# Performance work log

Measured on AMD Instinct MI355X. Metric: run time of the kernel, lower is better.

Reference implementation:

```python
import jax, jax.numpy as jnp
import numpy as np

B, L, H, C, K, S = 8, 336, 192, 321, 16, 8
H2 = H // 2 + 1            # rfft bins of pred_len
OUT = H2 * (2 * K + 1)     # FilterFactory out_dim


def _instance_norm(t):
    mu = t.mean(-1, keepdims=True)
    tc = t - mu
    std = jnp.sqrt((tc * tc).mean(-1, keepdims=True) + 1e-8)
    return tc / std, mu, std


def setup_inputs() -> dict:
    key = jax.random.key(0)
    ks = jax.random.split(key, 16)
    x = jax.random.normal(ks[0], (B, L, C), jnp.float32)
    y_hat = jax.random.normal(ks[1], (B, H, C), jnp.float32)
    leader_ids = jax.random.randint(ks[2], (B, C, K), 0, C)
    shift = jax.random.randint(ks[3], (B, C, K), 0, L)
    r = jax.random.normal(ks[4], (B, C, K), jnp.float32)
    temperature = jnp.ones((1,), jnp.float32)
    sl = 1.0 / np.sqrt(L)
    cls_w = jax.random.uniform(ks[5], (S, L), jnp.float32, -sl, sl)
    cls_bias = jax.random.uniform(ks[6], (S,), jnp.float32, -sl, sl)
    ss = 1.0 / np.sqrt(S)
    basic_state = jax.random.uniform(ks[7], (C, S), jnp.float32, -ss, ss)
    sk = 1.0 / np.sqrt(K)
    mh_w = jax.random.uniform(ks[8], (S, K * OUT), jnp.float32, -sk, sk)
    mh_b = jax.random.uniform(ks[9], (S, OUT), jnp.float32, -sk, sk)
    sm = 1.0 / np.sqrt(3 * H2)
    mix_w_real = jax.random.uniform(ks[10], (H2, 3 * H2), jnp.float32, -sm, sm)
    mix_w_imag = jax.random.uniform(ks[11], (H2, 3 * H2), jnp.float32, -sm, sm)
    mix_b_real = jax.random.uniform(ks[12], (H2,), jnp.float32, -sm, sm)
    mix_b_imag = jax.random.uniform(ks[13], (H2,), jnp.float32, -sm, sm)
    return dict(x=x, y_hat=y_hat, leader_ids=leader_ids, shift=shift, r=r,
                temperature=temperature, cls_w=cls_w, cls_bias=cls_bias,
                basic_state=basic_state, mh_w=mh_w, mh_b=mh_b,
                mix_w_real=mix_w_real, mix_w_imag=mix_w_imag,
                mix_b_real=mix_b_real, mix_b_imag=mix_b_imag)


def reference(x, y_hat, leader_ids, shift, r, temperature, cls_w, cls_bias,
              basic_state, mh_w, mh_b, mix_w_real, mix_w_imag,
              mix_b_real, mix_b_imag):
    xc = jnp.transpose(x, (0, 2, 1))        # [B,C,L]
    yh = jnp.transpose(y_hat, (0, 2, 1))    # [B,C,H]
    xn, mu, std = _instance_norm(xc)
    yhn = (yh - mu) / std

    # ---- shifted leader gather (no-grad region in original) ----
    seq = jnp.concatenate([xn, yhn], -1)                                      # [B,C,L+H]
    lead = jnp.take_along_axis(seq[:, None], leader_ids[..., None], axis=2)   # [B,C,K,L+H]
    idx = jnp.arange(L, L + H)[None, None, None, :] - shift[..., None]        # [B,C,K,H]
    seq_shifted = jnp.take_along_axis(lead, idx, axis=-1)
    seq_shifted = jax.lax.stop_gradient(seq_shifted * jnp.sign(r)[..., None])

    # ---- temperature softmax over [1, |r|] ----
    ones = jnp.ones((xc.shape[0], C, 1), xc.dtype)
    rw = jax.nn.softmax(jnp.concatenate([ones, jnp.abs(r)], -1) / temperature, axis=-1)
    corr_feat = rw[..., 1:]                                                   # [B,C,K]

    # ---- FilterFactory: state-routed filters ----
    p = jax.nn.softmax(cls_bias + basic_state + jnp.einsum('bcl,sl->bcs', xc, cls_w), axis=-1)
    w = jnp.einsum('bcs,so->bco', p, mh_w).reshape(-1, C, K, OUT)
    b = jnp.einsum('bcs,so->bco', p, mh_b)
    filt = (jnp.einsum('bck,bcko->bco', corr_feat, w) + b).reshape(-1, C, 2 * K + 1, H2)

    # ---- FFT filter mixing ----
    yf = jnp.fft.rfft(yhn)                                  # [B,C,H2] complex64
    sf = jnp.fft.rfft(seq_shifted) * filt[:, :, :K]         # [B,C,K,H2]
    df = (sf - yf[:, :, None]) * filt[:, :, K:-1]
    yf2 = yf * filt[:, :, -1]
    mix_in = jnp.concatenate([sf.sum(2), df.sum(2), yf2], -1)  # [B,C,3*H2]
    mix_w = mix_w_real + 1j * mix_w_imag
    mix_b = mix_b_real + 1j * mix_b_imag
    y = yhn + jnp.fft.irfft(mix_in @ mix_w.T + mix_b, n=H)
    y = y * std + mu
    return jnp.transpose(y, (0, 2, 1))                       # [B,H,C]
```

## Files before the change

### kernel.cpp

```cpp
#include <hip/hip_runtime.h>
#include <math.h>

#define B_ 8
#define L_ 336
#define H_ 192
#define C_ 321
#define K_ 16
#define S_ 8
#define H2_ 97
#define OUT_ 3201
#define SEQLEN_ 528
#define BC_ (B_ * C_)
#define JD_ 136
#define MIXJ_ 291
#define NP_ 208
#define MPAD_ 43712
#define NBLK_ 683
#define KF_ 160
#define MPADF_ 2576
#define NPADF_ 3264
#define KMX_ 608
#define NMX_ 208
#define KIR_ 224
#define NIR_ 192

typedef float v2f __attribute__((ext_vector_type(2)));
typedef float v4f __attribute__((ext_vector_type(4)));
typedef __attribute__((ext_vector_type(8))) short bf16x8;
typedef __attribute__((ext_vector_type(4))) float f32x4;

#define TWO_PI_F 6.283185307179586f

static constexpr size_t OFF_SEQ    = 0;
static constexpr size_t OFF_MU     = OFF_SEQ + (size_t)BC_ * SEQLEN_;
static constexpr size_t OFF_STD    = OFF_MU + BC_;
static constexpr size_t OFF_BPHI   = (OFF_STD + BC_ + 3) & ~(size_t)3;
static constexpr size_t OFF_BPLO   = OFF_BPHI + (size_t)NP_ * 192 / 2;
static constexpr size_t OFF_UHI    = (OFF_BPLO + (size_t)NP_ * 192 / 2 + 3) & ~(size_t)3;
static constexpr size_t OFF_ULO    = OFF_UHI + (size_t)MPADF_ * KF_ / 2;
static constexpr size_t OFF_W2HI   = OFF_ULO + (size_t)MPADF_ * KF_ / 2;
static constexpr size_t OFF_W2LO   = OFF_W2HI + (size_t)NPADF_ * KF_ / 2;
static constexpr size_t OFF_ROWS   = OFF_W2LO + (size_t)NPADF_ * KF_ / 2;
static constexpr size_t OFF_ROWSLO = OFF_ROWS + (size_t)MPAD_ * 192 / 2;
static constexpr size_t OFF_F      = OFF_ROWSLO + (size_t)MPAD_ * 192 / 2;
static constexpr size_t OFF_FILT   = OFF_ROWS;
static constexpr size_t OFF_MWHI   = OFF_F + (size_t)MPAD_ * NP_;
static constexpr size_t OFF_MWLO   = OFF_MWHI + (size_t)NMX_ * KMX_ / 2;
static constexpr size_t OFF_THI    = OFF_MWLO + (size_t)NMX_ * KMX_ / 2;
static constexpr size_t OFF_TLO    = OFF_THI + (size_t)NIR_ * KIR_ / 2;
static constexpr size_t OFF_MXHI   = OFF_TLO + (size_t)NIR_ * KIR_ / 2;
static constexpr size_t OFF_MXLO   = OFF_MXHI + (size_t)MPADF_ * KMX_ / 2;
static constexpr size_t OFF_ZHI    = OFF_MXLO + (size_t)MPADF_ * KMX_ / 2;
static constexpr size_t OFF_ZLO    = OFF_ZHI + (size_t)MPADF_ * KIR_ / 2;
static constexpr size_t OFF_Y      = OFF_ZLO + (size_t)MPADF_ * KIR_ / 2;

__device__ inline void split_bf16(float v, unsigned short& hh, unsigned short& ll) {
  unsigned u = __float_as_uint(v);
  unsigned hb = (u + 0x7FFFu + ((u >> 16) & 1u)) & 0xFFFF0000u;
  float fh = __uint_as_float(hb);
  float fl = v - fh;
  unsigned u2 = __float_as_uint(fl);
  unsigned lb = (u2 + 0x7FFFu + ((u2 >> 16) & 1u)) >> 16;
  hh = (unsigned short)(hb >> 16);
  ll = (unsigned short)lb;
}

__launch_bounds__(256)
__global__ void kStats(const float* __restrict__ x, const float* __restrict__ cls_w,
                       const float* __restrict__ cls_bias,
                       const float* __restrict__ basic_state, const float* __restrict__ r,
                       const float* __restrict__ temperature,
                       float* __restrict__ mu, float* __restrict__ stdv,
                       unsigned short* __restrict__ uhi, unsigned short* __restrict__ ulo) {
  __shared__ float part[4][10][64];
  __shared__ float sp[64][S_];
  __shared__ float scf[64][K_];

  int b = blockIdx.x;
  int cb = blockIdx.y * 64;
  int lane = threadIdx.x & 63;
  int wv = threadIdx.x >> 6;
  int c = cb + lane;
  bool cok = c < C_;

  float sum = 0.f, sumsq = 0.f, a[S_];
#pragma unroll
  for (int s = 0; s < S_; s++) a[s] = 0.f;
  if (cok) {
    for (int l = wv * 84; l < wv * 84 + 84; l++) {
      float v = x[((size_t)b * L_ + l) * C_ + c];
      sum += v;
      sumsq = fmaf(v, v, sumsq);
#pragma unroll
      for (int s = 0; s < S_; s++) a[s] = fmaf(v, cls_w[s * L_ + l], a[s]);
    }
  }
  part[wv][0][lane] = sum;
  part[wv][1][lane] = sumsq;
#pragma unroll
  for (int s = 0; s < S_; s++) part[wv][2 + s][lane] = a[s];
  __syncthreads();

  if (threadIdx.x < 64 && cok) {
    float s0 = 0.f, s1 = 0.f, ac[S_];
#pragma unroll
    for (int s = 0; s < S_; s++) ac[s] = 0.f;
#pragma unroll
    for (int w = 0; w < 4; w++) {
      s0 += part[w][0][lane];
      s1 += part[w][1][lane];
#pragma unroll
      for (int s = 0; s < S_; s++) ac[s] += part[w][2 + s][lane];
    }
    float m = s0 * (1.f / L_);
    float var = fmaxf(s1 * (1.f / L_) - m * m, 0.f);
    float sd = sqrtf(var + 1e-8f);
    int bc = b * C_ + c;
    mu[bc] = m;
    stdv[bc] = sd;

    float lg[S_], mx = -1e30f;
#pragma unroll
    for (int s = 0; s < S_; s++) {
      lg[s] = ac[s] + cls_bias[s] + basic_state[c * S_ + s];
      mx = fmaxf(mx, lg[s]);
    }
    float den = 0.f;
#pragma unroll
    for (int s = 0; s < S_; s++) { float e = expf(lg[s] - mx); lg[s] = e; den += e; }
    float iden = 1.f / den;
#pragma unroll
    for (int s = 0; s < S_; s++) sp[lane][s] = lg[s] * iden;

    float it = 1.f / temperature[0];
    float aa[K_], am = it;
#pragma unroll
    for (int k = 0; k < K_; k++) {
      aa[k] = fabsf(r[(size_t)bc * K_ + k]) * it;
      am = fmaxf(am, aa[k]);
    }
    float den2 = expf(it - am);
#pragma unroll
    for (int k = 0; k < K_; k++) { float e = expf(aa[k] - am); aa[k] = e; den2 += e; }
    float iden2 = 1.f / den2;
#pragma unroll
    for (int k = 0; k < K_; k++) scf[lane][k] = aa[k] * iden2;
  }
  __syncthreads();

  for (int idx = threadIdx.x; idx < 64 * KF_; idx += 256) {
    int ci = idx / KF_;
    int j = idx - ci * KF_;
    if (cb + ci < C_) {
      float v = 0.f;
      if (j < JD_) {
        int s = j / 17;
        int t = j - s * 17;
        v = sp[ci][s];
        if (t < K_) v *= scf[ci][t];
      }
      unsigned short hh, ll;
      split_bf16(v, hh, ll);
      size_t row = (size_t)(b * C_ + cb + ci) * KF_ + j;
      uhi[row] = hh;
      ulo[row] = ll;
    }
  }
}

__launch_bounds__(256)
__global__ void kSeqT(const float* __restrict__ x, const float* __restrict__ y_hat,
                      const float* __restrict__ mu, const float* __restrict__ stdv,
                      float* __restrict__ seq) {
  __shared__ float tile[32][33];
  int b = blockIdx.x;
  int cb = blockIdx.y * 32;
  int tb = blockIdx.z * 32;
  int ci = threadIdx.x & 31;
  int q8 = threadIdx.x >> 5;
  int c = cb + ci;
  float m = 0.f, is = 0.f;
  if (c < C_) {
    m = mu[b * C_ + c];
    is = 1.f / stdv[b * C_ + c];
  }
#pragma unroll
  for (int q = 0; q < 4; q++) {
    int tt = q8 + q * 8;
    int t = tb + tt;
    float v = 0.f;
    if (c < C_ && t < SEQLEN_)
      v = (t < L_) ? x[((size_t)b * L_ + t) * C_ + c]
                   : y_hat[((size_t)b * H_ + (t - L_)) * C_ + c];
    tile[ci][tt] = (v - m) * is;
  }
  __syncthreads();
#pragma unroll
  for (int q = 0; q < 4; q++) {
    int cc = cb + q8 + q * 8;
    int t = tb + ci;
    if (cc < C_ && t < SEQLEN_)
      seq[((size_t)b * C_ + cc) * SEQLEN_ + t] = tile[q8 + q * 8][ci];
  }
}

__global__ void kPackB(unsigned short* __restrict__ bhi, unsigned short* __restrict__ blo) {
  int idx = blockIdx.x * 256 + threadIdx.x;
  if (idx >= NP_ * 192) return;
  int n = idx / 192;
  int h = idx - n * 192;
  float val = 0.f;
  if (n < H2_) {
    int ph = (n * h) % 192;
    val = cosf((TWO_PI_F / 192.f) * (float)ph);
  } else if (n >= 104 && n < 104 + H2_) {
    int ph = ((n - 104) * h) % 192;
    val = -sinf((TWO_PI_F / 192.f) * (float)ph);
  }
  unsigned short hh, ll;
  split_bf16(val, hh, ll);
  bhi[idx] = hh;
  blo[idx] = ll;
}

__global__ void kPackW2(const float* __restrict__ mh_w, const float* __restrict__ mh_b,
                        unsigned short* __restrict__ w2hi, unsigned short* __restrict__ w2lo) {
  int idx = blockIdx.x * 256 + threadIdx.x;
  if (idx >= NPADF_ * KF_) return;
  int n = idx / KF_;
  int k = idx - n * KF_;
  float v = 0.f;
  if (n < OUT_ && k < JD_) {
    int s = k / 17;
    int t = k - s * 17;
    v = (t < K_) ? mh_w[(size_t)s * (K_ * OUT_) + (size_t)t * OUT_ + n]
                 : mh_b[(size_t)s * OUT_ + n];
  }
  unsigned short hh, ll;
  split_bf16(v, hh, ll);
  w2hi[idx] = hh;
  w2lo[idx] = ll;
}

__global__ void kPackMixW2(const float* __restrict__ mwr, const float* __restrict__ mwi,
                           const float* __restrict__ mbr, const float* __restrict__ mbi,
                           unsigned short* __restrict__ mwhi, unsigned short* __restrict__ mwlo) {
  int idx = blockIdx.x * 256 + threadIdx.x;
  if (idx >= NMX_ * KMX_) return;
  int n = idx / KMX_;
  int k = idx - n * KMX_;
  float v = 0.f;
  if (n < H2_) {
    int g = n;
    if (k < MIXJ_) v = mwr[(size_t)g * MIXJ_ + k];
    else if (k < 2 * MIXJ_) v = -mwi[(size_t)g * MIXJ_ + (k - MIXJ_)];
    else if (k == 2 * MIXJ_) v = mbr[g];
  } else if (n >= 104 && n < 104 + H2_) {
    int g = n - 104;
    if (k < MIXJ_) v = mwi[(size_t)g * MIXJ_ + k];
    else if (k < 2 * MIXJ_) v = mwr[(size_t)g * MIXJ_ + (k - MIXJ_)];
    else if (k == 2 * MIXJ_) v = mbi[g];
  }
  unsigned short hh, ll;
  split_bf16(v, hh, ll);
  mwhi[idx] = hh;
  mwlo[idx] = ll;
}

__global__ void kPackT(unsigned short* __restrict__ thi, unsigned short* __restrict__ tlo) {
  int idx = blockIdx.x * 256 + threadIdx.x;
  if (idx >= NIR_ * KIR_) return;
  int h = idx / KIR_;
  int k = idx - h * KIR_;
  float v = 0.f;
  if (k < H2_) {
    int f = k;
    float w = (f == 0 || f == 96) ? (1.f / 192.f) : (2.f / 192.f);
    int ph = (f * h) % 192;
    v = w * cosf((TWO_PI_F / 192.f) * (float)ph);
  } else if (k >= 104 && k < 104 + H2_) {
    int f = k - 104;
    if (f != 0 && f != 96) {
      int ph = (f * h) % 192;
      v = -(2.f / 192.f) * sinf((TWO_PI_F / 192.f) * (float)ph);
    }
  }
  unsigned short hh, ll;
  split_bf16(v, hh, ll);
  thi[idx] = hh;
  tlo[idx] = ll;
}

__launch_bounds__(128)
__global__ void kGather(const float* __restrict__ seq, const int* __restrict__ lead,
                        const int* __restrict__ shiftv, const float* __restrict__ r,
                        unsigned short* __restrict__ rhi, unsigned short* __restrict__ rlo) {
  int bc = blockIdx.x;
  int b = bc / C_;
  int lane = threadIdx.x;
#pragma unroll 1
  for (int k = 0; k < 17; k++) {
    float sg;
    const float* src;
    if (k < K_) {
      int ld = lead[(size_t)bc * K_ + k];
      int sh = shiftv[(size_t)bc * K_ + k];
      float rv = r[(size_t)bc * K_ + k];
      sg = (rv > 0.f) ? 1.f : ((rv < 0.f) ? -1.f : 0.f);
      src = seq + ((size_t)b * C_ + ld) * SEQLEN_ + (L_ - sh);
    } else {
      sg = 1.f;
      src = seq + (size_t)bc * SEQLEN_ + L_;
    }
    size_t mrow = (size_t)(bc * 17 + k) * 192;
#pragma unroll
    for (int p = 0; p < 2; p++) {
      int h = lane + p * 128;
      if (h < H_) {
        float v = src[h] * sg;
        unsigned short hh, ll;
        split_bf16(v, hh, ll);
        rhi[mrow + h] = hh;
        rlo[mrow + h] = ll;
      }
    }
  }
}

__launch_bounds__(256)
__global__ void kDFT(const unsigned short* __restrict__ rhi,
                     const unsigned short* __restrict__ rlo,
                     const unsigned short* __restrict__ bhi,
                     const unsigned short* __restrict__ blo,
                     float* __restrict__ F) {
  __shared__ __align__(16) unsigned short Bs[52 * 512];
  int tid = threadIdx.x;
  int wv = tid >> 6;
  int lane = tid & 63;
  int m0 = blockIdx.x * 64 + wv * 16;
  int row = lane & 15;
  int kg = lane >> 4;

  f32x4 acc[13];
#pragma unroll
  for (int nt = 0; nt < 13; nt++) acc[nt] = (f32x4){0.f, 0.f, 0.f, 0.f};

  const unsigned short* Ahb = rhi + (size_t)(m0 + row) * 192 + kg * 8;
  const unsigned short* Alb = rlo + (size_t)(m0 + row) * 192 + kg * 8;

#pragma unroll 1
  for (int part = 0; part < 3; part++) {
    __syncthreads();
    for (int s = tid >> 6; s < 52; s += 4) {
      int plane = s & 1;
      int ntks = s >> 1;
      int nt = ntks >> 1;
      int ks2 = ntks & 1;
      const unsigned short* src = (plane ? blo : bhi)
          + (size_t)(nt * 16 + row) * 192 + part * 64 + ks2 * 32 + kg * 8;
      *(bf16x8*)(Bs + s * 512 + lane * 8) = *(const bf16x8*)src;
    }
    __syncthreads();
#pragma unroll
    for (int ks2 = 0; ks2 < 2; ks2++) {
      int ksg = part * 2 + ks2;
      bf16x8 ah = *(const bf16x8*)(Ahb + ksg * 32);
      bf16x8 al = *(const bf16x8*)(Alb + ksg * 32);
#pragma unroll
      for (int nt = 0; nt < 13; nt++) {
        bf16x8 bh = *(const bf16x8*)(Bs + ((nt * 2 + ks2) * 2 + 0) * 512 + lane * 8);
        bf16x8 bl = *(const bf16x8*)(Bs + ((nt * 2 + ks2) * 2 + 1) * 512 + lane * 8);
        acc[nt] = __builtin_amdgcn_mfma_f32_16x16x32_bf16(ah, bh, acc[nt], 0, 0, 0);
        acc[nt] = __builtin_amdgcn_mfma_f32_16x16x32_bf16(ah, bl, acc[nt], 0, 0, 0);
        acc[nt] = __builtin_amdgcn_mfma_f32_16x16x32_bf16(al, bh, acc[nt], 0, 0, 0);
      }
    }
  }

  int crow0 = m0 + kg * 4;
#pragma unroll
  for (int nt = 0; nt < 13; nt++) {
#pragma unroll
    for (int rr = 0; rr < 4; rr++) {
      F[(size_t)(crow0 + rr) * NP_ + nt * 16 + row] = acc[nt][rr];
    }
  }
}

__launch_bounds__(256)
__global__ void kFiltMM(const unsigned short* __restrict__ uhi,
                        const unsigned short* __restrict__ ulo,
                        const unsigned short* __restrict__ w2hi,
                        const unsigned short* __restrict__ w2lo,
                        float* __restrict__ filt) {
  __shared__ __align__(16) unsigned short Ws[40 * 512];
  int tid = threadIdx.x;
  int wv = tid >> 6;
  int lane = tid & 63;
  int m0 = (blockIdx.y * 4 + wv) * 16;
  int n0 = blockIdx.x * 64;
  int col = lane & 15;
  int kg = lane >> 4;

  for (int s = tid >> 6; s < 40; s += 4) {
    int plane = s & 1;
    int ntk = s >> 1;
    int nt = ntk / 5;
    int ksi = ntk - nt * 5;
    const unsigned short* src = (plane ? w2lo : w2hi)
        + (size_t)(n0 + nt * 16 + col) * KF_ + ksi * 32 + kg * 8;
    *(bf16x8*)(Ws + s * 512 + lane * 8) = *(const bf16x8*)src;
  }
  __syncthreads();

  f32x4 acc[4];
#pragma unroll
  for (int nt = 0; nt < 4; nt++) acc[nt] = (f32x4){0.f, 0.f, 0.f, 0.f};

  int mrow = (m0 + col < MPADF_) ? (m0 + col) : (MPADF_ - 1);
  const unsigned short* Ah = uhi + (size_t)mrow * KF_ + kg * 8;
  const unsigned short* Al = ulo + (size_t)mrow * KF_ + kg * 8;

#pragma unroll
  for (int ks = 0; ks < 5; ks++) {
    bf16x8 ah = *(const bf16x8*)(Ah + ks * 32);
    bf16x8 al = *(const bf16x8*)(Al + ks * 32);
#pragma unroll
    for (int nt = 0; nt < 4; nt++) {
      bf16x8 bh = *(const bf16x8*)(Ws + ((nt * 5 + ks) * 2 + 0) * 512 + lane * 8);
      bf16x8 bl = *(const bf16x8*)(Ws + ((nt * 5 + ks) * 2 + 1) * 512 + lane * 8);
      acc[nt] = __builtin_amdgcn_mfma_f32_16x16x32_bf16(ah, bh, acc[nt], 0, 0, 0);
      acc[nt] = __builtin_amdgcn_mfma_f32_16x16x32_bf16(ah, bl, acc[nt], 0, 0, 0);
      acc[nt] = __builtin_amdgcn_mfma_f32_16x16x32_bf16(al, bh, acc[nt], 0, 0, 0);
    }
  }

  int crow0 = m0 + kg * 4;
#pragma unroll
  for (int nt = 0; nt < 4; nt++) {
    int o = n0 + nt * 16 + col;
    if (o < OUT_) {
#pragma unroll
      for (int rr = 0; rr < 4; rr++) {
        int m = crow0 + rr;
        if (m < BC_) filt[(size_t)m * OUT_ + o] = acc[nt][rr];
      }
    }
  }
}

__launch_bounds__(128)
__global__ void kCombine(const float* __restrict__ F, const float* __restrict__ filt,
                         unsigned short* __restrict__ mxhi, unsigned short* __restrict__ mxlo) {
  int bc = blockIdx.x;
  int ff = threadIdx.x;
  size_t mrowK = (size_t)bc * KMX_;

  if (ff < H2_) {
    float Fre[17], Fim[17];
#pragma unroll
    for (int k = 0; k < 17; k++) {
      size_t mr = (size_t)(bc * 17 + k) * NP_;
      Fre[k] = F[mr + ff];
      Fim[k] = F[mr + 104 + ff];
    }
    const float* fb = filt + (size_t)bc * OUT_;
    float yfR = Fre[16], yfI = Fim[16];
    float S1r = 0.f, S1i = 0.f, S2r = 0.f, S2i = 0.f, sg2 = 0.f;
#pragma unroll
    for (int k = 0; k < K_; k++) {
      float g1 = fb[k * H2_ + ff];
      float g2 = fb[(K_ + k) * H2_ + ff];
      float g12 = g1 * g2;
      S1r = fmaf(Fre[k], g1, S1r);
      S1i = fmaf(Fim[k], g1, S1i);
      S2r = fmaf(Fre[k], g12, S2r);
      S2i = fmaf(Fim[k], g12, S2i);
      sg2 += g2;
    }
    S2r = fmaf(-yfR, sg2, S2r);
    S2i = fmaf(-yfI, sg2, S2i);
    float g3 = fb[32 * H2_ + ff];
    float vals[6] = {S1r, S2r, yfR * g3, S1i, S2i, yfI * g3};
#pragma unroll
    for (int q = 0; q < 6; q++) {
      unsigned short hh, ll;
      split_bf16(vals[q], hh, ll);
      mxhi[mrowK + q * H2_ + ff] = hh;
      mxlo[mrowK + q * H2_ + ff] = ll;
    }
  } else if (ff == H2_) {
    mxhi[mrowK + 2 * MIXJ_] = 0x3F80;
    mxlo[mrowK + 2 * MIXJ_] = 0;
  } else if (ff >= 98 && ff < 98 + (KMX_ - 583)) {
    int k = 583 + (ff - 98);
    mxhi[mrowK + k] = 0;
    mxlo[mrowK + k] = 0;
  }
}

__launch_bounds__(256)
__global__ void kMixMM(const unsigned short* __restrict__ mxhi,
                       const unsigned short* __restrict__ mxlo,
                       const unsigned short* __restrict__ mwhi,
                       const unsigned short* __restrict__ mwlo,
                       unsigned short* __restrict__ zhi, unsigned short* __restrict__ zlo) {
  __shared__ __align__(16) unsigned short Bs[38 * 512];
  int tid = threadIdx.x;
  int wv = tid >> 6;
  int lane = tid & 63;
  int nt = blockIdx.x;
  int m0 = (blockIdx.y * 4 + wv) * 16;
  int row = lane & 15;
  int kg = lane >> 4;

  for (int s = wv; s < 38; s += 4) {
    int plane = s & 1;
    int ks = s >> 1;
    const unsigned short* src = (plane ? mwlo : mwhi)
        + (size_t)(nt * 16 + row) * KMX_ + ks * 32 + kg * 8;
    *(bf16x8*)(Bs + s * 512 + lane * 8) = *(const bf16x8*)src;
  }
  __syncthreads();

  if (m0 >= MPADF_) return;

  f32x4 acc = (f32x4){0.f, 0.f, 0.f, 0.f};
  const unsigned short* Ah = mxhi + (size_t)(m0 + row) * KMX_ + kg * 8;
  const unsigned short* Al = mxlo + (size_t)(m0 + row) * KMX_ + kg * 8;

#pragma unroll
  for (int ks = 0; ks < 19; ks++) {
    bf16x8 ah = *(const bf16x8*)(Ah + ks * 32);
    bf16x8 al = *(const bf16x8*)(Al + ks * 32);
    bf16x8 bh = *(const bf16x8*)(Bs + (ks * 2 + 0) * 512 + lane * 8);
    bf16x8 bl = *(const bf16x8*)(Bs + (ks * 2 + 1) * 512 + lane * 8);
    acc = __builtin_amdgcn_mfma_f32_16x16x32_bf16(ah, bh, acc, 0, 0, 0);
    acc = __builtin_amdgcn_mfma_f32_16x16x32_bf16(ah, bl, acc, 0, 0, 0);
    acc = __builtin_amdgcn_mfma_f32_16x16x32_bf16(al, bh, acc, 0, 0, 0);
  }

  int crow0 = m0 + kg * 4;
#pragma unroll
  for (int rr = 0; rr < 4; rr++) {
    unsigned short hh, ll;
    split_bf16(acc[rr], hh, ll);
    zhi[(size_t)(crow0 + rr) * KIR_ + nt * 16 + row] = hh;
    zlo[(size_t)(crow0 + rr) * KIR_ + nt * 16 + row] = ll;
  }
  if (nt == 12) {
    for (int cc = 208 + kg; cc < KIR_; cc += 4) {
      zhi[(size_t)(m0 + row) * KIR_ + cc] = 0;
      zlo[(size_t)(m0 + row) * KIR_ + cc] = 0;
    }
  }
}

__launch_bounds__(256)
__global__ void kIrfft(const unsigned short* __restrict__ zhi,
                       const unsigned short* __restrict__ zlo,
                       const unsigned short* __restrict__ thi,
                       const unsigned short* __restrict__ tlo,
                       float* __restrict__ y) {
  __shared__ __align__(16) unsigned short Bs[14 * 512];
  int tid = threadIdx.x;
  int wv = tid >> 6;
  int lane = tid & 63;
  int nt = blockIdx.x;
  int m0 = (blockIdx.y * 4 + wv) * 16;
  int row = lane & 15;
  int kg = lane >> 4;

  for (int s = wv; s < 14; s += 4) {
    int plane = s & 1;
    int ks = s >> 1;
    const unsigned short* src = (plane ? tlo : thi)
        + (size_t)(nt * 16 + row) * KIR_ + ks * 32 + kg * 8;
    *(bf16x8*)(Bs + s * 512 + lane * 8) = *(const bf16x8*)src;
  }
  __syncthreads();

  if (m0 >= MPADF_) return;

  f32x4 acc = (f32x4){0.f, 0.f, 0.f, 0.f};
  const unsigned short* Ah = zhi + (size_t)(m0 + row) * KIR_ + kg * 8;
  const unsigned short* Al = zlo + (size_t)(m0 + row) * KIR_ + kg * 8;

#pragma unroll
  for (int ks = 0; ks < 7; ks++) {
    bf16x8 ah = *(const bf16x8*)(Ah + ks * 32);
    bf16x8 al = *(const bf16x8*)(Al + ks * 32);
    bf16x8 bh = *(const bf16x8*)(Bs + (ks * 2 + 0) * 512 + lane * 8);
    bf16x8 bl = *(const bf16x8*)(Bs + (ks * 2 + 1) * 512 + lane * 8);
    acc = __builtin_amdgcn_mfma_f32_16x16x32_bf16(ah, bh, acc, 0, 0, 0);
    acc = __builtin_amdgcn_mfma_f32_16x16x32_bf16(ah, bl, acc, 0, 0, 0);
    acc = __builtin_amdgcn_mfma_f32_16x16x32_bf16(al, bh, acc, 0, 0, 0);
  }

  int crow0 = m0 + kg * 4;
#pragma unroll
  for (int rr = 0; rr < 4; rr++) {
    y[(size_t)(crow0 + rr) * NIR_ + nt * 16 + row] = acc[rr];
  }
}

__launch_bounds__(256)
__global__ void kEpi(const float* __restrict__ y, const float* __restrict__ seq,
                     const float* __restrict__ mu, const float* __restrict__ stdv,
                     float* __restrict__ out) {
  __shared__ float tile[32][33];
  int b = blockIdx.x;
  int cb = blockIdx.y * 32;
  int hb = blockIdx.z * 32;
  int lane5 = threadIdx.x & 31;
  int q8 = threadIdx.x >> 5;

#pragma unroll
  for (int q = 0; q < 4; q++) {
    int cc = q8 + q * 8;
    int c = cb + cc;
    float v = 0.f;
    if (c < C_) {
      size_t bc = (size_t)b * C_ + c;
      v = y[bc * NIR_ + hb + lane5] + seq[bc * SEQLEN_ + L_ + hb + lane5];
    }
    tile[cc][lane5] = v;
  }
  __syncthreads();

  int c2 = cb + lane5;
  if (c2 < C_) {
    float m = mu[b * C_ + c2];
    float sd = stdv[b * C_ + c2];
#pragma unroll
    for (int q = 0; q < 4; q++) {
      int hh = q8 + q * 8;
      out[((size_t)b * H_ + hb + hh) * C_ + c2] = fmaf(tile[lane5][hh], sd, m);
    }
  }
}

extern "C" void kernel_launch(void* const* d_in, const int* in_sizes, int n_in,
                              void* d_out, int out_size, void* d_ws, size_t ws_size,
                              hipStream_t stream) {
  const float* x           = (const float*)d_in[0];
  const float* y_hat       = (const float*)d_in[1];
  const int*   lead        = (const int*)d_in[2];
  const int*   shiftv      = (const int*)d_in[3];
  const float* r           = (const float*)d_in[4];
  const float* temperature = (const float*)d_in[5];
  const float* cls_w       = (const float*)d_in[6];
  const float* cls_bias    = (const float*)d_in[7];
  const float* basic_state = (const float*)d_in[8];
  const float* mh_w        = (const float*)d_in[9];
  const float* mh_b        = (const float*)d_in[10];
  const float* mwr         = (const float*)d_in[11];
  const float* mwi         = (const float*)d_in[12];
  const float* mbr         = (const float*)d_in[13];
  const float* mbi         = (const float*)d_in[14];
  float* out = (float*)d_out;
  float* ws  = (float*)d_ws;

  unsigned short* bphi = (unsigned short*)(ws + OFF_BPHI);
  unsigned short* bplo = (unsigned short*)(ws + OFF_BPLO);
  unsigned short* uhi  = (unsigned short*)(ws + OFF_UHI);
  unsigned short* ulo  = (unsigned short*)(ws + OFF_ULO);
  unsigned short* w2hi = (unsigned short*)(ws + OFF_W2HI);
  unsigned short* w2lo = (unsigned short*)(ws + OFF_W2LO);
  unsigned short* rhi  = (unsigned short*)(ws + OFF_ROWS);
  unsigned short* rlo  = (unsigned short*)(ws + OFF_ROWSLO);
  unsigned short* mwhi = (unsigned short*)(ws + OFF_MWHI);
  unsigned short* mwlo = (unsigned short*)(ws + OFF_MWLO);
  unsigned short* thi  = (unsigned short*)(ws + OFF_THI);
  unsigned short* tlo  = (unsigned short*)(ws + OFF_TLO);
  unsigned short* mxhi = (unsigned short*)(ws + OFF_MXHI);
  unsigned short* mxlo = (unsigned short*)(ws + OFF_MXLO);
  unsigned short* zhi  = (unsigned short*)(ws + OFF_ZHI);
  unsigned short* zlo  = (unsigned short*)(ws + OFF_ZLO);

  dim3 gS(B_, 6);
  kStats<<<gS, 256, 0, stream>>>(x, cls_w, cls_bias, basic_state, r, temperature,
                                 ws + OFF_MU, ws + OFF_STD, uhi, ulo);

  dim3 gT(B_, 11, 17);
  kSeqT<<<gT, 256, 0, stream>>>(x, y_hat, ws + OFF_MU, ws + OFF_STD, ws + OFF_SEQ);

  kPackB<<<(NP_ * 192 + 255) / 256, 256, 0, stream>>>(bphi, bplo);
  kPackW2<<<(NPADF_ * KF_ + 255) / 256, 256, 0, stream>>>(mh_w, mh_b, w2hi, w2lo);
  kPackMixW2<<<(NMX_ * KMX_ + 255) / 256, 256, 0, stream>>>(mwr, mwi, mbr, mbi, mwhi, mwlo);
  kPackT<<<(NIR_ * KIR_ + 255) / 256, 256, 0, stream>>>(thi, tlo);

  kGather<<<BC_, 128, 0, stream>>>(ws + OFF_SEQ, lead, shiftv, r, rhi, rlo);

  kDFT<<<NBLK_, 256, 0, stream>>>(rhi, rlo, bphi, bplo, ws + OFF_F);

  dim3 gFM(NPADF_ / 64, (MPADF_ / 16 + 3) / 4);
  kFiltMM<<<gFM, 256, 0, stream>>>(uhi, ulo, w2hi, w2lo, ws + OFF_FILT);

  kCombine<<<BC_, 128, 0, stream>>>(ws + OFF_F, ws + OFF_FILT, mxhi, mxlo);

  dim3 gMX(13, 41);
  kMixMM<<<gMX, 256, 0, stream>>>(mxhi, mxlo, mwhi, mwlo, zhi, zlo);

  dim3 gIR(12, 41);
  kIrfft<<<gIR, 256, 0, stream>>>(zhi, zlo, thi, tlo, ws + OFF_Y);

  dim3 gE(B_, 11, 6);
  kEpi<<<gE, 256, 0, stream>>>(ws + OFF_Y, ws + OFF_SEQ, ws + OFF_MU, ws + OFF_STD, out);
}
```

Baseline: 227.0 us.

## Fuse stats with seq transpose, gather into DFT, irfft into epilogue, pack kernels

```diff
diff --git a/kernel.cpp b/kernel.cpp
--- a/kernel.cpp
+++ b/kernel.cpp
@@ -14,8 +14,7 @@
 #define JD_ 136
 #define MIXJ_ 291
 #define NP_ 208
-#define MPAD_ 43712
-#define NBLK_ 683
+#define MROWS_ 43656
 #define KF_ 160
 #define MPADF_ 2576
 #define NPADF_ 3264
@@ -31,28 +30,25 @@
 
 #define TWO_PI_F 6.283185307179586f
 
-static constexpr size_t OFF_SEQ    = 0;
-static constexpr size_t OFF_MU     = OFF_SEQ + (size_t)BC_ * SEQLEN_;
-static constexpr size_t OFF_STD    = OFF_MU + BC_;
-static constexpr size_t OFF_BPHI   = (OFF_STD + BC_ + 3) & ~(size_t)3;
-static constexpr size_t OFF_BPLO   = OFF_BPHI + (size_t)NP_ * 192 / 2;
-static constexpr size_t OFF_UHI    = (OFF_BPLO + (size_t)NP_ * 192 / 2 + 3) & ~(size_t)3;
-static constexpr size_t OFF_ULO    = OFF_UHI + (size_t)MPADF_ * KF_ / 2;
-static constexpr size_t OFF_W2HI   = OFF_ULO + (size_t)MPADF_ * KF_ / 2;
-static constexpr size_t OFF_W2LO   = OFF_W2HI + (size_t)NPADF_ * KF_ / 2;
-static constexpr size_t OFF_ROWS   = OFF_W2LO + (size_t)NPADF_ * KF_ / 2;
-static constexpr size_t OFF_ROWSLO = OFF_ROWS + (size_t)MPAD_ * 192 / 2;
-static constexpr size_t OFF_F      = OFF_ROWSLO + (size_t)MPAD_ * 192 / 2;
-static constexpr size_t OFF_FILT   = OFF_ROWS;
-static constexpr size_t OFF_MWHI   = OFF_F + (size_t)MPAD_ * NP_;
-static constexpr size_t OFF_MWLO   = OFF_MWHI + (size_t)NMX_ * KMX_ / 2;
-static constexpr size_t OFF_THI    = OFF_MWLO + (size_t)NMX_ * KMX_ / 2;
-static constexpr size_t OFF_TLO    = OFF_THI + (size_t)NIR_ * KIR_ / 2;
-static constexpr size_t OFF_MXHI   = OFF_TLO + (size_t)NIR_ * KIR_ / 2;
-static constexpr size_t OFF_MXLO   = OFF_MXHI + (size_t)MPADF_ * KMX_ / 2;
-static constexpr size_t OFF_ZHI    = OFF_MXLO + (size_t)MPADF_ * KMX_ / 2;
-static constexpr size_t OFF_ZLO    = OFF_ZHI + (size_t)MPADF_ * KIR_ / 2;
-static constexpr size_t OFF_Y      = OFF_ZLO + (size_t)MPADF_ * KIR_ / 2;
+static constexpr size_t OFF_SEQ  = 0;
+static constexpr size_t OFF_MU   = OFF_SEQ + (size_t)BC_ * SEQLEN_;
+static constexpr size_t OFF_STD  = OFF_MU + BC_;
+static constexpr size_t OFF_BPHI = (OFF_STD + BC_ + 3) & ~(size_t)3;
+static constexpr size_t OFF_BPLO = OFF_BPHI + (size_t)NP_ * 192 / 2;
+static constexpr size_t OFF_UHI  = OFF_BPLO + (size_t)NP_ * 192 / 2;
+static constexpr size_t OFF_ULO  = OFF_UHI + (size_t)MPADF_ * KF_ / 2;
+static constexpr size_t OFF_W2HI = OFF_ULO + (size_t)MPADF_ * KF_ / 2;
+static constexpr size_t OFF_W2LO = OFF_W2HI + (size_t)NPADF_ * KF_ / 2;
+static constexpr size_t OFF_MWHI = OFF_W2LO + (size_t)NPADF_ * KF_ / 2;
+static constexpr size_t OFF_MWLO = OFF_MWHI + (size_t)NMX_ * KMX_ / 2;
+static constexpr size_t OFF_THI  = OFF_MWLO + (size_t)NMX_ * KMX_ / 2;
+static constexpr size_t OFF_TLO  = OFF_THI + (size_t)NIR_ * KIR_ / 2;
+static constexpr size_t OFF_F    = OFF_TLO + (size_t)NIR_ * KIR_ / 2;
+static constexpr size_t OFF_FILT = OFF_F + (size_t)MROWS_ * NP_;
+static constexpr size_t OFF_MXHI = OFF_FILT + (size_t)BC_ * OUT_;
+static constexpr size_t OFF_MXLO = OFF_MXHI + (size_t)MPADF_ * KMX_ / 2;
+static constexpr size_t OFF_ZHI  = OFF_MXLO + (size_t)MPADF_ * KMX_ / 2;
+static constexpr size_t OFF_ZLO  = OFF_ZHI + (size_t)MPADF_ * KIR_ / 2;
 
 __device__ inline void split_bf16(float v, unsigned short& hh, unsigned short& ll) {
   unsigned u = __float_as_uint(v);
@@ -66,15 +62,18 @@
 }
 
 __launch_bounds__(256)
-__global__ void kStats(const float* __restrict__ x, const float* __restrict__ cls_w,
-                       const float* __restrict__ cls_bias,
-                       const float* __restrict__ basic_state, const float* __restrict__ r,
-                       const float* __restrict__ temperature,
-                       float* __restrict__ mu, float* __restrict__ stdv,
-                       unsigned short* __restrict__ uhi, unsigned short* __restrict__ ulo) {
+__global__ void kPre(const float* __restrict__ x, const float* __restrict__ y_hat,
+                     const float* __restrict__ cls_w, const float* __restrict__ cls_bias,
+                     const float* __restrict__ basic_state, const float* __restrict__ r,
+                     const float* __restrict__ temperature,
+                     float* __restrict__ mu, float* __restrict__ stdv,
+                     unsigned short* __restrict__ uhi, unsigned short* __restrict__ ulo,
+                     float* __restrict__ seq) {
   __shared__ float part[4][10][64];
   __shared__ float sp[64][S_];
   __shared__ float scf[64][K_];
+  __shared__ float smu[64], sis[64];
+  __shared__ float tile[64][33];
 
   int b = blockIdx.x;
   int cb = blockIdx.y * 64;
@@ -118,6 +117,8 @@
     int bc = b * C_ + c;
     mu[bc] = m;
     stdv[bc] = sd;
+    smu[lane] = m;
+    sis[lane] = 1.f / sd;
 
     float lg[S_], mx = -1e30f;
 #pragma unroll
@@ -161,197 +162,174 @@
       }
       unsigned short hh, ll;
       split_bf16(v, hh, ll);
-      size_t row = (size_t)(b * C_ + cb + ci) * KF_ + j;
-      uhi[row] = hh;
-      ulo[row] = ll;
-    }
-  }
-}
-
-__launch_bounds__(256)
-__global__ void kSeqT(const float* __restrict__ x, const float* __restrict__ y_hat,
-                      const float* __restrict__ mu, const float* __restrict__ stdv,
-                      float* __restrict__ seq) {
-  __shared__ float tile[32][33];
-  int b = blockIdx.x;
-  int cb = blockIdx.y * 32;
-  int tb = blockIdx.z * 32;
-  int ci = threadIdx.x & 31;
-  int q8 = threadIdx.x >> 5;
-  int c = cb + ci;
-  float m = 0.f, is = 0.f;
-  if (c < C_) {
-    m = mu[b * C_ + c];
-    is = 1.f / stdv[b * C_ + c];
-  }
-#pragma unroll
-  for (int q = 0; q < 4; q++) {
-    int tt = q8 + q * 8;
-    int t = tb + tt;
-    float v = 0.f;
-    if (c < C_ && t < SEQLEN_)
-      v = (t < L_) ? x[((size_t)b * L_ + t) * C_ + c]
-                   : y_hat[((size_t)b * H_ + (t - L_)) * C_ + c];
-    tile[ci][tt] = (v - m) * is;
-  }
-  __syncthreads();
-#pragma unroll
-  for (int q = 0; q < 4; q++) {
-    int cc = cb + q8 + q * 8;
-    int t = tb + ci;
-    if (cc < C_ && t < SEQLEN_)
-      seq[((size_t)b * C_ + cc) * SEQLEN_ + t] = tile[q8 + q * 8][ci];
-  }
-}
-
-__global__ void kPackB(unsigned short* __restrict__ bhi, unsigned short* __restrict__ blo) {
-  int idx = blockIdx.x * 256 + threadIdx.x;
-  if (idx >= NP_ * 192) return;
-  int n = idx / 192;
-  int h = idx - n * 192;
-  float val = 0.f;
-  if (n < H2_) {
-    int ph = (n * h) % 192;
-    val = cosf((TWO_PI_F / 192.f) * (float)ph);
-  } else if (n >= 104 && n < 104 + H2_) {
-    int ph = ((n - 104) * h) % 192;
-    val = -sinf((TWO_PI_F / 192.f) * (float)ph);
-  }
-  unsigned short hh, ll;
-  split_bf16(val, hh, ll);
-  bhi[idx] = hh;
-  blo[idx] = ll;
-}
-
-__global__ void kPackW2(const float* __restrict__ mh_w, const float* __restrict__ mh_b,
-                        unsigned short* __restrict__ w2hi, unsigned short* __restrict__ w2lo) {
-  int idx = blockIdx.x * 256 + threadIdx.x;
-  if (idx >= NPADF_ * KF_) return;
-  int n = idx / KF_;
-  int k = idx - n * KF_;
+      size_t rowi = (size_t)(b * C_ + cb + ci) * KF_ + j;
+      uhi[rowi] = hh;
+      ulo[rowi] = ll;
+    }
+  }
+
+  for (int t0 = 0; t0 < SEQLEN_; t0 += 32) {
+    int nmax = (SEQLEN_ - t0 < 32) ? (SEQLEN_ - t0) : 32;
+    for (int tt = wv; tt < nmax; tt += 4) {
+      int t = t0 + tt;
+      float v = 0.f;
+      if (cok) {
+        v = (t < L_) ? x[((size_t)b * L_ + t) * C_ + c]
+                     : y_hat[((size_t)b * H_ + (t - L_)) * C_ + c];
+        v = (v - smu[lane]) * sis[lane];
+      }
+      tile[lane][tt] = v;
+    }
+    __syncthreads();
+    int tpos = threadIdx.x & 31;
+    if (tpos < nmax) {
+      for (int ci = (int)(threadIdx.x >> 5); ci < 64; ci += 8) {
+        if (cb + ci < C_)
+          seq[((size_t)b * C_ + cb + ci) * SEQLEN_ + t0 + tpos] = tile[ci][tpos];
+      }
+    }
+    __syncthreads();
+  }
+}
+
+__global__ void kPackAll(const float* __restrict__ mh_w, const float* __restrict__ mh_b,
+                         const float* __restrict__ mwr, const float* __restrict__ mwi,
+                         const float* __restrict__ mbr, const float* __restrict__ mbi,
+                         unsigned short* __restrict__ bhi, unsigned short* __restrict__ blo,
+                         unsigned short* __restrict__ w2hi, unsigned short* __restrict__ w2lo,
+                         unsigned short* __restrict__ mwhi, unsigned short* __restrict__ mwlo,
+                         unsigned short* __restrict__ thi, unsigned short* __restrict__ tlo) {
+  const int T1 = NP_ * 192;
+  const int T2 = T1 + NPADF_ * KF_;
+  const int T3 = T2 + NMX_ * KMX_;
+  const int T4 = T3 + NIR_ * KIR_;
+  int i = blockIdx.x * 256 + threadIdx.x;
+  if (i >= T4) return;
   float v = 0.f;
-  if (n < OUT_ && k < JD_) {
-    int s = k / 17;
-    int t = k - s * 17;
-    v = (t < K_) ? mh_w[(size_t)s * (K_ * OUT_) + (size_t)t * OUT_ + n]
-                 : mh_b[(size_t)s * OUT_ + n];
+  unsigned short* dhi;
+  unsigned short* dlo;
+  int didx;
+  if (i < T1) {
+    int n = i / 192, h = i - n * 192;
+    if (n < H2_) {
+      int ph = (n * h) % 192;
+      v = cosf((TWO_PI_F / 192.f) * (float)ph);
+    } else if (n >= 104 && n < 104 + H2_) {
+      int ph = ((n - 104) * h) % 192;
+      v = -sinf((TWO_PI_F / 192.f) * (float)ph);
+    }
+    dhi = bhi; dlo = blo; didx = i;
+  } else if (i < T2) {
+    int idx = i - T1;
+    int n = idx / KF_, k = idx - n * KF_;
+    if (n < OUT_ && k < JD_) {
+      int s = k / 17, t = k - s * 17;
+      v = (t < K_) ? mh_w[(size_t)s * (K_ * OUT_) + (size_t)t * OUT_ + n]
+                   : mh_b[(size_t)s * OUT_ + n];
+    }
+    dhi = w2hi; dlo = w2lo; didx = idx;
+  } else if (i < T3) {
+    int idx = i - T2;
+    int n = idx / KMX_, k = idx - n * KMX_;
+    if (n < H2_) {
+      int g = n;
+      if (k < MIXJ_) v = mwr[(size_t)g * MIXJ_ + k];
+      else if (k < 2 * MIXJ_) v = -mwi[(size_t)g * MIXJ_ + (k - MIXJ_)];
+      else if (k == 2 * MIXJ_) v = mbr[g];
+    } else if (n >= 104 && n < 104 + H2_) {
+      int g = n - 104;
+      if (k < MIXJ_) v = mwi[(size_t)g * MIXJ_ + k];
+      else if (k < 2 * MIXJ_) v = mwr[(size_t)g * MIXJ_ + (k - MIXJ_)];
+      else if (k == 2 * MIXJ_) v = mbi[g];
+    }
+    dhi = mwhi; dlo = mwlo; didx = idx;
+  } else {
+    int idx = i - T3;
+    int h = idx / KIR_, k = idx - h * KIR_;
+    if (k < H2_) {
+      int f = k;
+      float w = (f == 0 || f == 96) ? (1.f / 192.f) : (2.f / 192.f);
+      int ph = (f * h) % 192;
+      v = w * cosf((TWO_PI_F / 192.f) * (float)ph);
+    } else if (k >= 104 && k < 104 + H2_) {
+      int f = k - 104;
+      if (f != 0 && f != 96) {
+        int ph = (f * h) % 192;
+        v = -(2.f / 192.f) * sinf((TWO_PI_F / 192.f) * (float)ph);
+      }
+    }
+    dhi = thi; dlo = tlo; didx = idx;
   }
   unsigned short hh, ll;
   split_bf16(v, hh, ll);
-  w2hi[idx] = hh;
-  w2lo[idx] = ll;
-}
-
-__global__ void kPackMixW2(const float* __restrict__ mwr, const float* __restrict__ mwi,
-                           const float* __restrict__ mbr, const float* __restrict__ mbi,
-                           unsigned short* __restrict__ mwhi, unsigned short* __restrict__ mwlo) {
-  int idx = blockIdx.x * 256 + threadIdx.x;
-  if (idx >= NMX_ * KMX_) return;
-  int n = idx / KMX_;
-  int k = idx - n * KMX_;
-  float v = 0.f;
-  if (n < H2_) {
-    int g = n;
-    if (k < MIXJ_) v = mwr[(size_t)g * MIXJ_ + k];
-    else if (k < 2 * MIXJ_) v = -mwi[(size_t)g * MIXJ_ + (k - MIXJ_)];
-    else if (k == 2 * MIXJ_) v = mbr[g];
-  } else if (n >= 104 && n < 104 + H2_) {
-    int g = n - 104;
-    if (k < MIXJ_) v = mwi[(size_t)g * MIXJ_ + k];
-    else if (k < 2 * MIXJ_) v = mwr[(size_t)g * MIXJ_ + (k - MIXJ_)];
-    else if (k == 2 * MIXJ_) v = mbi[g];
-  }
-  unsigned short hh, ll;
-  split_bf16(v, hh, ll);
-  mwhi[idx] = hh;
-  mwlo[idx] = ll;
-}
-
-__global__ void kPackT(unsigned short* __restrict__ thi, unsigned short* __restrict__ tlo) {
-  int idx = blockIdx.x * 256 + threadIdx.x;
-  if (idx >= NIR_ * KIR_) return;
-  int h = idx / KIR_;
-  int k = idx - h * KIR_;
-  float v = 0.f;
-  if (k < H2_) {
-    int f = k;
-    float w = (f == 0 || f == 96) ? (1.f / 192.f) : (2.f / 192.f);
-    int ph = (f * h) % 192;
-    v = w * cosf((TWO_PI_F / 192.f) * (float)ph);
-  } else if (k >= 104 && k < 104 + H2_) {
-    int f = k - 104;
-    if (f != 0 && f != 96) {
-      int ph = (f * h) % 192;
-      v = -(2.f / 192.f) * sinf((TWO_PI_F / 192.f) * (float)ph);
-    }
-  }
-  unsigned short hh, ll;
-  split_bf16(v, hh, ll);
-  thi[idx] = hh;
-  tlo[idx] = ll;
-}
-
-__launch_bounds__(128)
-__global__ void kGather(const float* __restrict__ seq, const int* __restrict__ lead,
-                        const int* __restrict__ shiftv, const float* __restrict__ r,
-                        unsigned short* __restrict__ rhi, unsigned short* __restrict__ rlo) {
-  int bc = blockIdx.x;
-  int b = bc / C_;
-  int lane = threadIdx.x;
-#pragma unroll 1
-  for (int k = 0; k < 17; k++) {
+  dhi[didx] = hh;
+  dlo[didx] = ll;
+}
+
+__launch_bounds__(320)
+__global__ void kGatherDFT(const float* __restrict__ seq, const int* __restrict__ lead,
+                           const int* __restrict__ shiftv, const float* __restrict__ r,
+                           const unsigned short* __restrict__ bhi,
+                           const unsigned short* __restrict__ blo,
+                           float* __restrict__ F) {
+  __shared__ __align__(16) unsigned short Ah[80 * 200];
+  __shared__ __align__(16) unsigned short Al[80 * 200];
+  __shared__ __align__(16) unsigned short Bs[52 * 512];
+  __shared__ int soff[68];
+  __shared__ float ssgn[68];
+
+  int tid = threadIdx.x;
+  int wv = tid >> 6;
+  int lane = tid & 63;
+  int bc0 = blockIdx.x * 4;
+
+  if (tid < 68) {
+    int lr = tid;
+    int bcl = lr / 17;
+    int k = lr - bcl * 17;
+    int bc = bc0 + bcl;
+    int b = bc / C_;
+    int off;
     float sg;
-    const float* src;
     if (k < K_) {
       int ld = lead[(size_t)bc * K_ + k];
       int sh = shiftv[(size_t)bc * K_ + k];
       float rv = r[(size_t)bc * K_ + k];
       sg = (rv > 0.f) ? 1.f : ((rv < 0.f) ? -1.f : 0.f);
-      src = seq + ((size_t)b * C_ + ld) * SEQLEN_ + (L_ - sh);
+      off = (b * C_ + ld) * SEQLEN_ + (L_ - sh);
     } else {
       sg = 1.f;
-      src = seq + (size_t)bc * SEQLEN_ + L_;
-    }
-    size_t mrow = (size_t)(bc * 17 + k) * 192;
-#pragma unroll
-    for (int p = 0; p < 2; p++) {
-      int h = lane + p * 128;
-      if (h < H_) {
-        float v = src[h] * sg;
-        unsigned short hh, ll;
-        split_bf16(v, hh, ll);
-        rhi[mrow + h] = hh;
-        rlo[mrow + h] = ll;
-      }
-    }
-  }
-}
-
-__launch_bounds__(256)
-__global__ void kDFT(const unsigned short* __restrict__ rhi,
-                     const unsigned short* __restrict__ rlo,
-                     const unsigned short* __restrict__ bhi,
-                     const unsigned short* __restrict__ blo,
-                     float* __restrict__ F) {
-  __shared__ __align__(16) unsigned short Bs[52 * 512];
-  int tid = threadIdx.x;
-  int wv = tid >> 6;
-  int lane = tid & 63;
-  int m0 = blockIdx.x * 64 + wv * 16;
+      off = bc * SEQLEN_ + L_;
+    }
+    soff[lr] = off;
+    ssgn[lr] = sg;
+  }
+  __syncthreads();
+
+  for (int idx = tid; idx < 68 * 192; idx += 320) {
+    int lr = idx / 192;
+    int h = idx - lr * 192;
+    float v = seq[soff[lr] + h] * ssgn[lr];
+    unsigned short hh, ll;
+    split_bf16(v, hh, ll);
+    Ah[lr * 200 + h] = hh;
+    Al[lr * 200 + h] = ll;
+  }
+  for (int i = 68 * 200 + tid; i < 80 * 200; i += 320) { Ah[i] = 0; Al[i] = 0; }
+
   int row = lane & 15;
   int kg = lane >> 4;
-
   f32x4 acc[13];
 #pragma unroll
   for (int nt = 0; nt < 13; nt++) acc[nt] = (f32x4){0.f, 0.f, 0.f, 0.f};
 
-  const unsigned short* Ahb = rhi + (size_t)(m0 + row) * 192 + kg * 8;
-  const unsigned short* Alb = rlo + (size_t)(m0 + row) * 192 + kg * 8;
+  const unsigned short* Abh = Ah + (wv * 16 + row) * 200 + kg * 8;
+  const unsigned short* Abl = Al + (wv * 16 + row) * 200 + kg * 8;
 
 #pragma unroll 1
   for (int part = 0; part < 3; part++) {
     __syncthreads();
-    for (int s = tid >> 6; s < 52; s += 4) {
+    for (int s = wv; s < 52; s += 5) {
       int plane = s & 1;
       int ntks = s >> 1;
       int nt = ntks >> 1;
@@ -364,8 +342,8 @@
 #pragma unroll
     for (int ks2 = 0; ks2 < 2; ks2++) {
       int ksg = part * 2 + ks2;
-      bf16x8 ah = *(const bf16x8*)(Ahb + ksg * 32);
-      bf16x8 al = *(const bf16x8*)(Alb + ksg * 32);
+      bf16x8 ah = *(const bf16x8*)(Abh + ksg * 32);
+      bf16x8 al = *(const bf16x8*)(Abl + ksg * 32);
 #pragma unroll
       for (int nt = 0; nt < 13; nt++) {
         bf16x8 bh = *(const bf16x8*)(Bs + ((nt * 2 + ks2) * 2 + 0) * 512 + lane * 8);
@@ -377,12 +355,14 @@
     }
   }
 
-  int crow0 = m0 + kg * 4;
+  int ml0 = wv * 16 + kg * 4;
 #pragma unroll
   for (int nt = 0; nt < 13; nt++) {
 #pragma unroll
     for (int rr = 0; rr < 4; rr++) {
-      F[(size_t)(crow0 + rr) * NP_ + nt * 16 + row] = acc[nt][rr];
+      int ml = ml0 + rr;
+      if (ml < 68)
+        F[((size_t)bc0 * 17 + ml) * NP_ + nt * 16 + row] = acc[nt][rr];
     }
   }
 }
@@ -402,7 +382,7 @@
   int col = lane & 15;
   int kg = lane >> 4;
 
-  for (int s = tid >> 6; s < 40; s += 4) {
+  for (int s = wv; s < 40; s += 4) {
     int plane = s & 1;
     int ntk = s >> 1;
     int nt = ntk / 5;
@@ -418,13 +398,13 @@
   for (int nt = 0; nt < 4; nt++) acc[nt] = (f32x4){0.f, 0.f, 0.f, 0.f};
 
   int mrow = (m0 + col < MPADF_) ? (m0 + col) : (MPADF_ - 1);
-  const unsigned short* Ah = uhi + (size_t)mrow * KF_ + kg * 8;
-  const unsigned short* Al = ulo + (size_t)mrow * KF_ + kg * 8;
+  const unsigned short* Ahp = uhi + (size_t)mrow * KF_ + kg * 8;
+  const unsigned short* Alp = ulo + (size_t)mrow * KF_ + kg * 8;
 
 #pragma unroll
   for (int ks = 0; ks < 5; ks++) {
-    bf16x8 ah = *(const bf16x8*)(Ah + ks * 32);
-    bf16x8 al = *(const bf16x8*)(Al + ks * 32);
+    bf16x8 ah = *(const bf16x8*)(Ahp + ks * 32);
+    bf16x8 al = *(const bf16x8*)(Alp + ks * 32);
 #pragma unroll
     for (int nt = 0; nt < 4; nt++) {
       bf16x8 bh = *(const bf16x8*)(Ws + ((nt * 5 + ks) * 2 + 0) * 512 + lane * 8);
@@ -526,13 +506,13 @@
   if (m0 >= MPADF_) return;
 
   f32x4 acc = (f32x4){0.f, 0.f, 0.f, 0.f};
-  const unsigned short* Ah = mxhi + (size_t)(m0 + row) * KMX_ + kg * 8;
-  const unsigned short* Al = mxlo + (size_t)(m0 + row) * KMX_ + kg * 8;
+  const unsigned short* Ahp = mxhi + (size_t)(m0 + row) * KMX_ + kg * 8;
+  const unsigned short* Alp = mxlo + (size_t)(m0 + row) * KMX_ + kg * 8;
 
 #pragma unroll
   for (int ks = 0; ks < 19; ks++) {
-    bf16x8 ah = *(const bf16x8*)(Ah + ks * 32);
-    bf16x8 al = *(const bf16x8*)(Al + ks * 32);
+    bf16x8 ah = *(const bf16x8*)(Ahp + ks * 32);
+    bf16x8 al = *(const bf16x8*)(Alp + ks * 32);
     bf16x8 bh = *(const bf16x8*)(Bs + (ks * 2 + 0) * 512 + lane * 8);
     bf16x8 bl = *(const bf16x8*)(Bs + (ks * 2 + 1) * 512 + lane * 8);
     acc = __builtin_amdgcn_mfma_f32_16x16x32_bf16(ah, bh, acc, 0, 0, 0);
@@ -557,17 +537,20 @@
 }
 
 __launch_bounds__(256)
-__global__ void kIrfft(const unsigned short* __restrict__ zhi,
-                       const unsigned short* __restrict__ zlo,
-                       const unsigned short* __restrict__ thi,
-                       const unsigned short* __restrict__ tlo,
-                       float* __restrict__ y) {
+__global__ void kIrfftEpi(const unsigned short* __restrict__ zhi,
+                          const unsigned short* __restrict__ zlo,
+                          const unsigned short* __restrict__ thi,
+                          const unsigned short* __restrict__ tlo,
+                          const float* __restrict__ seq, const float* __restrict__ mu,
+                          const float* __restrict__ stdv, float* __restrict__ out) {
   __shared__ __align__(16) unsigned short Bs[14 * 512];
+  __shared__ float ytile[64][17];
   int tid = threadIdx.x;
   int wv = tid >> 6;
   int lane = tid & 63;
   int nt = blockIdx.x;
-  int m0 = (blockIdx.y * 4 + wv) * 16;
+  int mblk = blockIdx.y * 64;
+  int m0 = mblk + wv * 16;
   int row = lane & 15;
   int kg = lane >> 4;
 
@@ -580,16 +563,15 @@
   }
   __syncthreads();
 
-  if (m0 >= MPADF_) return;
-
   f32x4 acc = (f32x4){0.f, 0.f, 0.f, 0.f};
-  const unsigned short* Ah = zhi + (size_t)(m0 + row) * KIR_ + kg * 8;
-  const unsigned short* Al = zlo + (size_t)(m0 + row) * KIR_ + kg * 8;
+  int ar = (m0 + row < MPADF_) ? (m0 + row) : (MPADF_ - 1);
+  const unsigned short* Ahp = zhi + (size_t)ar * KIR_ + kg * 8;
+  const unsigned short* Alp = zlo + (size_t)ar * KIR_ + kg * 8;
 
 #pragma unroll
   for (int ks = 0; ks < 7; ks++) {
-    bf16x8 ah = *(const bf16x8*)(Ah + ks * 32);
-    bf16x8 al = *(const bf16x8*)(Al + ks * 32);
+    bf16x8 ah = *(const bf16x8*)(Ahp + ks * 32);
+    bf16x8 al = *(const bf16x8*)(Alp + ks * 32);
     bf16x8 bh = *(const bf16x8*)(Bs + (ks * 2 + 0) * 512 + lane * 8);
     bf16x8 bl = *(const bf16x8*)(Bs + (ks * 2 + 1) * 512 + lane * 8);
     acc = __builtin_amdgcn_mfma_f32_16x16x32_bf16(ah, bh, acc, 0, 0, 0);
@@ -597,45 +579,23 @@
     acc = __builtin_amdgcn_mfma_f32_16x16x32_bf16(al, bh, acc, 0, 0, 0);
   }
 
-  int crow0 = m0 + kg * 4;
-#pragma unroll
-  for (int rr = 0; rr < 4; rr++) {
-    y[(size_t)(crow0 + rr) * NIR_ + nt * 16 + row] = acc[rr];
-  }
-}
-
-__launch_bounds__(256)
-__global__ void kEpi(const float* __restrict__ y, const float* __restrict__ seq,
-                     const float* __restrict__ mu, const float* __restrict__ stdv,
-                     float* __restrict__ out) {
-  __shared__ float tile[32][33];
-  int b = blockIdx.x;
-  int cb = blockIdx.y * 32;
-  int hb = blockIdx.z * 32;
-  int lane5 = threadIdx.x & 31;
-  int q8 = threadIdx.x >> 5;
-
-#pragma unroll
-  for (int q = 0; q < 4; q++) {
-    int cc = q8 + q * 8;
-    int c = cb + cc;
-    float v = 0.f;
-    if (c < C_) {
-      size_t bc = (size_t)b * C_ + c;
-      v = y[bc * NIR_ + hb + lane5] + seq[bc * SEQLEN_ + L_ + hb + lane5];
-    }
-    tile[cc][lane5] = v;
-  }
+  int ml0 = wv * 16 + kg * 4;
+#pragma unroll
+  for (int rr = 0; rr < 4; rr++) ytile[ml0 + rr][row] = acc[rr];
   __syncthreads();
 
-  int c2 = cb + lane5;
-  if (c2 < C_) {
-    float m = mu[b * C_ + c2];
-    float sd = stdv[b * C_ + c2];
+  int ml = tid & 63;
+  int bc = mblk + ml;
+  if (bc < BC_) {
+    int b = bc / C_;
+    int c = bc - b * C_;
+    float m = mu[bc], sd = stdv[bc];
+    const float* sq = seq + (size_t)bc * SEQLEN_ + L_;
 #pragma unroll
     for (int q = 0; q < 4; q++) {
-      int hh = q8 + q * 8;
-      out[((size_t)b * H_ + hb + hh) * C_ + c2] = fmaf(tile[lane5][hh], sd, m);
+      int hl = (tid >> 6) * 4 + q;
+      int h = nt * 16 + hl;
+      out[((size_t)b * H_ + h) * C_ + c] = fmaf(sq[h] + ytile[ml][hl], sd, m);
     }
   }
 }
@@ -667,8 +627,6 @@
   unsigned short* ulo  = (unsigned short*)(ws + OFF_ULO);
   unsigned short* w2hi = (unsigned short*)(ws + OFF_W2HI);
   unsigned short* w2lo = (unsigned short*)(ws + OFF_W2LO);
-  unsigned short* rhi  = (unsigned short*)(ws + OFF_ROWS);
-  unsigned short* rlo  = (unsigned short*)(ws + OFF_ROWSLO);
   unsigned short* mwhi = (unsigned short*)(ws + OFF_MWHI);
   unsigned short* mwlo = (unsigned short*)(ws + OFF_MWLO);
   unsigned short* thi  = (unsigned short*)(ws + OFF_THI);
@@ -678,21 +636,18 @@
   unsigned short* zhi  = (unsigned short*)(ws + OFF_ZHI);
   unsigned short* zlo  = (unsigned short*)(ws + OFF_ZLO);
 
-  dim3 gS(B_, 6);
-  kStats<<<gS, 256, 0, stream>>>(x, cls_w, cls_bias, basic_state, r, temperature,
-                                 ws + OFF_MU, ws + OFF_STD, uhi, ulo);
-
-  dim3 gT(B_, 11, 17);
-  kSeqT<<<gT, 256, 0, stream>>>(x, y_hat, ws + OFF_MU, ws + OFF_STD, ws + OFF_SEQ);
-
-  kPackB<<<(NP_ * 192 + 255) / 256, 256, 0, stream>>>(bphi, bplo);
-  kPackW2<<<(NPADF_ * KF_ + 255) / 256, 256, 0, stream>>>(mh_w, mh_b, w2hi, w2lo);
-  kPackMixW2<<<(NMX_ * KMX_ + 255) / 256, 256, 0, stream>>>(mwr, mwi, mbr, mbi, mwhi, mwlo);
-  kPackT<<<(NIR_ * KIR_ + 255) / 256, 256, 0, stream>>>(thi, tlo);
-
-  kGather<<<BC_, 128, 0, stream>>>(ws + OFF_SEQ, lead, shiftv, r, rhi, rlo);
-
-  kDFT<<<NBLK_, 256, 0, stream>>>(rhi, rlo, bphi, bplo, ws + OFF_F);
+  dim3 gP(B_, 6);
+  kPre<<<gP, 256, 0, stream>>>(x, y_hat, cls_w, cls_bias, basic_state, r,
+                               temperature, ws + OFF_MU, ws + OFF_STD,
+                               uhi, ulo, ws + OFF_SEQ);
+
+  const int TPK = NP_ * 192 + NPADF_ * KF_ + NMX_ * KMX_ + NIR_ * KIR_;
+  kPackAll<<<(TPK + 255) / 256, 256, 0, stream>>>(mh_w, mh_b, mwr, mwi, mbr, mbi,
+                                                  bphi, bplo, w2hi, w2lo,
+                                                  mwhi, mwlo, thi, tlo);
+
+  kGatherDFT<<<BC_ / 4, 320, 0, stream>>>(ws + OFF_SEQ, lead, shiftv, r,
+                                          bphi, bplo, ws + OFF_F);
 
   dim3 gFM(NPADF_ / 64, (MPADF_ / 16 + 3) / 4);
   kFiltMM<<<gFM, 256, 0, stream>>>(uhi, ulo, w2hi, w2lo, ws + OFF_FILT);
@@ -703,8 +658,6 @@
   kMixMM<<<gMX, 256, 0, stream>>>(mxhi, mxlo, mwhi, mwlo, zhi, zlo);
 
   dim3 gIR(12, 41);
-  kIrfft<<<gIR, 256, 0, stream>>>(zhi, zlo, thi, tlo, ws + OFF_Y);
-
-  dim3 gE(B_, 11, 6);
-  kEpi<<<gE, 256, 0, stream>>>(ws + OFF_Y, ws + OFF_SEQ, ws + OFF_MU, ws + OFF_STD, out);
-}
+  kIrfftEpi<<<gIR, 256, 0, stream>>>(zhi, zlo, thi, tlo, ws + OFF_SEQ,
+                                     ws + OFF_MU, ws + OFF_STD, out);
+}
```

New measurement: 278.6 us. +22.7%, slower.
